# Kernel optimization log

Hardware: AMD Instinct MI355X
Metric: run time of the kernel (lower is better)

The kernel has to match this reference:

```python
import jax, jax.numpy as jnp
import numpy as np

N = 50000
NEG_SLOPE = 0.2


def leaky_relu(x, slope=NEG_SLOPE):
    return jnp.where(x >= 0, x, slope * x)


def gat_conv(x, edge_index, W, a_src, a_dst, bias):
    """PyG GATConv, heads=1, add_self_loops=True.
    x: [N, Fin], edge_index: [2, E] (row 0 = source j, row 1 = target i),
    W: [Fin, Fout], a_src/a_dst: [Fout], bias: [Fout].
    """
    n = x.shape[0]
    # add self loops
    loops = jnp.arange(n, dtype=edge_index.dtype)
    src = jnp.concatenate([edge_index[0], loops])
    dst = jnp.concatenate([edge_index[1], loops])

    xw = x @ W                       # [N, Fout]
    alpha_src = xw @ a_src           # [N]
    alpha_dst = xw @ a_dst           # [N]

    e = leaky_relu(alpha_src[src] + alpha_dst[dst])   # [E+N]
    # segment softmax over edges sharing the same target node
    m = jax.ops.segment_max(e, dst, num_segments=n)   # [N]
    ex = jnp.exp(e - m[dst])
    denom = jax.ops.segment_sum(ex, dst, num_segments=n)  # [N] (>0 via self loops)
    att = ex / denom[dst]                              # [E+N]

    msgs = att[:, None] * xw[src]                      # [E+N, Fout]
    out = jax.ops.segment_sum(msgs, dst, num_segments=n)
    return out + bias


def setup_inputs() -> dict:
    key = jax.random.key(0)
    ks = jax.random.split(key, 12)
    E = 800000
    Fin, H, Fout = 128, 256, 128
    x = jax.random.normal(ks[0], (N, Fin), dtype=jnp.float32)
    edge_index = jax.random.randint(ks[1], (2, E), 0, N, dtype=jnp.int64)
    s = 0.1
    W1 = jax.random.normal(ks[2], (Fin, H), dtype=jnp.float32) * s
    a1_src = jax.random.normal(ks[3], (H,), dtype=jnp.float32) * s
    a1_dst = jax.random.normal(ks[4], (H,), dtype=jnp.float32) * s
    b1 = jax.random.normal(ks[5], (H,), dtype=jnp.float32) * s
    W2 = jax.random.normal(ks[6], (H, Fout), dtype=jnp.float32) * s
    a2_src = jax.random.normal(ks[7], (Fout,), dtype=jnp.float32) * s
    a2_dst = jax.random.normal(ks[8], (Fout,), dtype=jnp.float32) * s
    b2 = jax.random.normal(ks[9], (Fout,), dtype=jnp.float32) * s
    return {"x": x, "edge_index": edge_index, "W1": W1, "a1_src": a1_src,
            "a1_dst": a1_dst, "b1": b1, "W2": W2, "a2_src": a2_src,
            "a2_dst": a2_dst, "b2": b2}


def reference(x, edge_index, W1, a1_src, a1_dst, b1, W2, a2_src, a2_dst, b2):
    h = jax.nn.relu(gat_conv(x, edge_index, W1, a1_src, a1_dst, b1))
    return gat_conv(h, edge_index, W2, a2_src, a2_dst, b2)
```

## Files before the change

kernel.cpp:

```cpp
#include <hip/hip_runtime.h>
#include <hip/hip_bf16.h>

typedef __attribute__((ext_vector_type(8))) short short8;
typedef __attribute__((ext_vector_type(4))) float floatx4;

#define CAP 8192
#define BIN_CH 2048
#define NPB 16

__device__ __forceinline__ float read_f(const void* p, long long i, int fp32m) {
  return fp32m ? ((const float*)p)[i] : (float)((const __hip_bfloat16*)p)[i];
}
__device__ __forceinline__ float bf2f(unsigned short u) {
  return __uint_as_float((unsigned)u << 16);
}
__device__ __forceinline__ unsigned short f2bf(float f) {
  const unsigned u = __float_as_uint(f);
  return (unsigned short)((u + 0x7fffu + ((u >> 16) & 1u)) >> 16);
}

__device__ __forceinline__ void pack_one(const void* W, unsigned short* Wp, int i,
                                         int K, int NOUT, int m) {
  const int k = i / NOUT, n = i - k * NOUT;
  const int ct = n >> 4, c = n & 15, ks = k >> 5, quad = (k >> 3) & 3, j = k & 7;
  Wp[(((ct * (K / 32) + ks) * 4 + quad) * 16 + c) * 8 + j] = f2bf(read_f(W, i, m));
}

__global__ __launch_bounds__(256) void prep_k(const void* __restrict__ x,
                                              const void* __restrict__ ei,
                                              const void* __restrict__ W1,
                                              const void* __restrict__ a1s,
                                              const void* __restrict__ a1d,
                                              const void* __restrict__ b1,
                                              const void* __restrict__ W2,
                                              const void* __restrict__ a2s,
                                              const void* __restrict__ a2d,
                                              const void* __restrict__ b2,
                                              unsigned short* __restrict__ Wp1,
                                              unsigned short* __restrict__ Wp2,
                                              float* __restrict__ w_as1, float* __restrict__ w_ad1,
                                              float* __restrict__ v_a2s, float* __restrict__ v_a2d,
                                              float* __restrict__ v_b1,  float* __restrict__ v_b2,
                                              int* __restrict__ bkcnt,
                                              int* __restrict__ flags) {
  __shared__ int fl_s[2];
  const int t = threadIdx.x, b = blockIdx.x;
  if (t < 64) {
    const unsigned short w = ((const unsigned short*)x)[t * 2];
    const int ef = (w >> 7) & 0xff;
    const bool bf_ok = (ef >= 90 && ef <= 140);
    const unsigned hi = ((const unsigned*)ei)[t * 2 + 1];
    const unsigned long long bm = __ballot(bf_ok);
    const unsigned long long zm = __ballot(hi == 0u);
    if (t == 0) {
      fl_s[0] = (bm == ~0ull) ? 0 : 1;
      fl_s[1] = (zm == ~0ull) ? 1 : 0;
      if (b == 0) { flags[0] = fl_s[0]; flags[1] = fl_s[1]; }
    }
  }
  __syncthreads();
  const int m = fl_s[0];

  if (b < 128) {
    pack_one(W1, Wp1, b * 256 + t, 128, 256, m);
  } else if (b < 256) {
    pack_one(W2, Wp2, (b - 128) * 256 + t, 256, 128, m);
  } else if (b == 256) {
    if (t < 128) {
      float sa = 0.f, sb = 0.f;
      for (int j = 0; j < 256; ++j) {
        const float w = read_f(W1, (long long)t * 256 + j, m);
        sa = fmaf(w, read_f(a1s, j, m), sa);
        sb = fmaf(w, read_f(a1d, j, m), sb);
      }
      w_as1[t] = sa;
      w_ad1[t] = sb;
    }
  } else if (b == 257) {
    if (t < 128) v_a2s[t] = read_f(a2s, t, m);
    else         v_a2d[t - 128] = read_f(a2d, t - 128, m);
  } else if (b == 258) {
    v_b1[t] = read_f(b1, t, m);
  } else {
    if (t < 128) v_b2[t] = read_f(b2, t, m);
    bkcnt[t] = 0;
  }
}

__device__ __forceinline__ void edge_sd(const void* ei, int e, int E, int i64m, int n,
                                        int& s, int& d) {
  if (e < E) {
    if (i64m) { s = (int)((const long long*)ei)[e]; d = (int)((const long long*)ei)[E + e]; }
    else      { s = ((const int*)ei)[e];            d = ((const int*)ei)[E + e]; }
  } else { s = d = e - E; }
  s = min(max(s, 0), n - 1);
  d = min(max(d, 0), n - 1);
}

__global__ __launch_bounds__(256) void front2_k(const void* __restrict__ x,
                                                const void* __restrict__ ei,
                                                const float* __restrict__ w_as1,
                                                const float* __restrict__ w_ad1,
                                                unsigned short* __restrict__ xb,
                                                float* __restrict__ as_, float* __restrict__ ad_,
                                                unsigned* __restrict__ bpool,
                                                int* __restrict__ bkcnt,
                                                int n, int E, int EN, int nbc) {
  __shared__ int fl_s[2];
  __shared__ unsigned stage[BIN_CH];
  __shared__ unsigned daddr[BIN_CH];
  __shared__ int shA[256], shB[256], shC[256], shD[256];
  __shared__ int vtot_s;
  const int t = threadIdx.x, b = blockIdx.x;

  if (t < 64) {
    const unsigned short w = ((const unsigned short*)x)[t * 2];
    const int ef = (w >> 7) & 0xff;
    const bool bf_ok = (ef >= 90 && ef <= 140);
    const unsigned hi = ((const unsigned*)ei)[t * 2 + 1];
    const unsigned long long bm = __ballot(bf_ok);
    const unsigned long long zm = __ballot(hi == 0u);
    if (t == 0) {
      fl_s[0] = (bm == ~0ull) ? 0 : 1;
      fl_s[1] = (zm == ~0ull) ? 1 : 0;
    }
  }
  __syncthreads();
  const int m = fl_s[0], i64m = fl_s[1];

  if (b < nbc) {
    const int gid = b * 256 + t;
    const int node = gid >> 6, lane = gid & 63;
    if (node >= n) return;
    const long long base = (long long)node * 128 + lane * 2;
    const float v0 = read_f(x, base, m), v1 = read_f(x, base + 1, m);
    ushort2 q;
    q.x = f2bf(v0); q.y = f2bf(v1);
    *(ushort2*)(xb + base) = q;
    float s1 = fmaf(v0, w_as1[lane * 2], v1 * w_as1[lane * 2 + 1]);
    float s2 = fmaf(v0, w_ad1[lane * 2], v1 * w_ad1[lane * 2 + 1]);
    for (int off = 32; off; off >>= 1) {
      s1 += __shfl_down(s1, off);
      s2 += __shfl_down(s2, off);
    }
    if (lane == 0) { as_[node] = s1; ad_[node] = s2; }
  } else {
    const int c0 = (b - nbc) * BIN_CH;
    int* bcnt_s = shA; int* boff_s = shB; int* gbase_s = shC; int* sd = shD;
    bcnt_s[t] = 0;
    __syncthreads();

    unsigned val[BIN_CH / 256];
    int buk[BIN_CH / 256];
#pragma unroll
    for (int i = 0; i < BIN_CH / 256; ++i) {
      const int e = c0 + i * 256 + t;
      if (e < EN) {
        int s, d;
        edge_sd(ei, e, E, i64m, n, s, d);
        buk[i] = d >> 8;
        val[i] = (unsigned)s | ((unsigned)(d & 255) << 16);
        atomicAdd(&bcnt_s[buk[i]], 1);
      } else buk[i] = -1;
    }
    __syncthreads();

    const int c = bcnt_s[t];
    sd[t] = c;
    __syncthreads();
    for (int off = 1; off < 256; off <<= 1) {
      const int v = (t >= off) ? sd[t - off] : 0;
      __syncthreads();
      sd[t] += v;
      __syncthreads();
    }
    boff_s[t] = sd[t] - c;
    if (t == 255) vtot_s = sd[255];
    gbase_s[t] = (c > 0) ? atomicAdd(&bkcnt[t], c) : 0;
    bcnt_s[t] = 0;
    __syncthreads();

#pragma unroll
    for (int i = 0; i < BIN_CH / 256; ++i) {
      if (buk[i] >= 0) {
        const int lp = atomicAdd(&bcnt_s[buk[i]], 1);
        const int si = boff_s[buk[i]] + lp;
        stage[si] = val[i];
        const int gp = gbase_s[buk[i]] + lp;
        daddr[si] = (gp < CAP) ? (unsigned)(buk[i] * CAP + gp) : 0xFFFFFFFFu;
      }
    }
    __syncthreads();

    const int vt = vtot_s;
    for (int idx = t; idx < vt; idx += 256)
      if (daddr[idx] != 0xFFFFFFFFu) bpool[daddr[idx]] = stage[idx];
  }
}

__global__ __launch_bounds__(1024) void bucket_csr_k(const unsigned* __restrict__ bpool,
                                                     const int* __restrict__ bkcnt,
                                                     const float* __restrict__ as_,
                                                     const float* __restrict__ ad_,
                                                     unsigned* __restrict__ csr32,
                                                     int* __restrict__ start_g,
                                                     int* __restrict__ deg_g,
                                                     float* __restrict__ r1_g, int n) {
  __shared__ int deg_s[256], cur_s[256], sd[256];
  __shared__ float dsum_s[256];
  const int t = threadIdx.x, b = blockIdx.x;
  int cnt = bkcnt[b];
  if (cnt > CAP) cnt = CAP;
  if (t < 256) { deg_s[t] = 0; dsum_s[t] = 0.f; }
  __syncthreads();
  for (int idx = t; idx < cnt; idx += 1024) {
    const unsigned v = bpool[b * CAP + idx];
    atomicAdd(&deg_s[(v >> 16) & 255], 1);
  }
  __syncthreads();
  const int dg = (t < 256) ? deg_s[t] : 0;
  if (t < 256) sd[t] = dg;
  __syncthreads();
  for (int off = 1; off < 256; off <<= 1) {
    const int v = (t < 256 && t >= off) ? sd[t - off] : 0;
    __syncthreads();
    if (t < 256) sd[t] += v;
    __syncthreads();
  }
  if (t < 256) {
    const int excl = sd[t] - dg;
    const int node = b * 256 + t;
    if (node < n) { start_g[node] = b * CAP + excl; deg_g[node] = dg; }
    cur_s[t] = excl;
  }
  __syncthreads();
  for (int idx = t; idx < cnt; idx += 1024) {
    const unsigned v = bpool[b * CAP + idx];
    const int dl = (v >> 16) & 255;
    const int s = (int)(v & 0xFFFFu);
    float val = as_[s] + ad_[b * 256 + dl];
    val = (val >= 0.f) ? val : 0.2f * val;
    const float w = __expf(fminf(val, 60.f));
    const unsigned short wb = f2bf(w);
    atomicAdd(&dsum_s[dl], bf2f(wb));
    const int p = atomicAdd(&cur_s[dl], 1);
    csr32[b * CAP + p] = (unsigned)s | ((unsigned)wb << 16);
  }
  __syncthreads();
  if (t < 256) {
    const int node = b * 256 + t;
    if (node < n) r1_g[node] = 1.f / fmaxf(dsum_s[t], 1e-30f);
  }
}

__device__ __forceinline__ void agg_node_w(const int start, const int end,
                                           const unsigned* __restrict__ csr32,
                                           const unsigned short* __restrict__ xw,
                                           const int lane, const float rnorm,
                                           float* acc, const unsigned e_first) {
  const int slot = lane >> 4, col = lane & 15;
#pragma unroll
  for (int c = 0; c < 8; ++c) acc[c] = 0.f;

  for (int base = start; base < end; base += 64) {
    const unsigned e_pre = (base == start) ? e_first
                         : ((base + lane < end) ? csr32[base + lane] : 0u);
    const int cnt = min(64, end - base);
    for (int j = 0; j < cnt; j += 8) {
      const int jj0 = j + slot, jj1 = j + 4 + slot;
      unsigned e0 = (unsigned)__shfl((int)e_pre, jj0);
      unsigned e1 = (unsigned)__shfl((int)e_pre, jj1);
      e0 = (jj0 < cnt) ? e0 : 0u;
      e1 = (jj1 < cnt) ? e1 : 0u;
      const int s0 = (int)(e0 & 0xFFFFu), s1 = (int)(e1 & 0xFFFFu);
      const float w0 = bf2f((unsigned short)(e0 >> 16));
      const float w1 = bf2f((unsigned short)(e1 >> 16));
      const short8 q0 = *(const short8*)(xw + (size_t)s0 * 128 + col * 8);
      const short8 q1 = *(const short8*)(xw + (size_t)s1 * 128 + col * 8);
#pragma unroll
      for (int c = 0; c < 8; ++c) {
        acc[c] = fmaf(w0, bf2f((unsigned short)q0[c]), acc[c]);
        acc[c] = fmaf(w1, bf2f((unsigned short)q1[c]), acc[c]);
      }
    }
  }
#pragma unroll
  for (int c = 0; c < 8; ++c) {
    acc[c] += __shfl_xor(acc[c], 16);
    acc[c] += __shfl_xor(acc[c], 32);
    acc[c] *= rnorm;
  }
}

__device__ __forceinline__ void agg_node2_p(const int start, const int end,
                                            const unsigned* __restrict__ csr32,
                                            const float* __restrict__ as2, const float adv,
                                            const unsigned short* __restrict__ xw,
                                            const int lane, const unsigned p_first,
                                            float* acc) {
  const int slot = lane >> 4, col = lane & 15;
  float dsum = 0.f;
#pragma unroll
  for (int c = 0; c < 8; ++c) acc[c] = 0.f;

  for (int base = start; base < end; base += 64) {
    unsigned p_pre;
    if (base == start) {
      p_pre = p_first;
    } else {
      p_pre = 0u;
      const int idx = base + lane;
      if (idx < end) {
        const int s = (int)(csr32[idx] & 0xFFFFu);
        float v = as2[s] + adv;
        v = (v >= 0.f) ? v : 0.2f * v;
        const unsigned short wb = f2bf(__expf(fminf(v, 60.f)));
        p_pre = (unsigned)s | ((unsigned)wb << 16);
      }
    }
    dsum += bf2f((unsigned short)(p_pre >> 16));
    const int cnt = min(64, end - base);
    for (int j = 0; j < cnt; j += 8) {
      const int jj0 = j + slot, jj1 = j + 4 + slot;
      unsigned e0 = (unsigned)__shfl((int)p_pre, jj0);
      unsigned e1 = (unsigned)__shfl((int)p_pre, jj1);
      e0 = (jj0 < cnt) ? e0 : 0u;
      e1 = (jj1 < cnt) ? e1 : 0u;
      const int s0 = (int)(e0 & 0xFFFFu), s1 = (int)(e1 & 0xFFFFu);
      const float w0 = bf2f((unsigned short)(e0 >> 16));
      const float w1 = bf2f((unsigned short)(e1 >> 16));
      const short8 q0 = *(const short8*)(xw + (size_t)s0 * 128 + col * 8);
      const short8 q1 = *(const short8*)(xw + (size_t)s1 * 128 + col * 8);
#pragma unroll
      for (int c = 0; c < 8; ++c) {
        acc[c] = fmaf(w0, bf2f((unsigned short)q0[c]), acc[c]);
        acc[c] = fmaf(w1, bf2f((unsigned short)q1[c]), acc[c]);
      }
    }
  }
  for (int off = 32; off; off >>= 1) dsum += __shfl_down(dsum, off);
  dsum = __shfl(dsum, 0);
  const float r = 1.f / fmaxf(dsum, 1e-30f);
#pragma unroll
  for (int c = 0; c < 8; ++c) {
    acc[c] += __shfl_xor(acc[c], 16);
    acc[c] += __shfl_xor(acc[c], 32);
    acc[c] *= r;
  }
}

#define LSTR 136
#define HSTR 264
__global__ __launch_bounds__(256, 8) void agg_gemm12_k(const int* __restrict__ start_g,
                                                       const int* __restrict__ deg_g,
                                                       const unsigned* __restrict__ csr32,
                                                       const float* __restrict__ r1_g,
                                                       const unsigned short* __restrict__ xb,
                                                       const unsigned short* __restrict__ Wp1,
                                                       const unsigned short* __restrict__ Wp2,
                                                       const float* __restrict__ v_b1,
                                                       const float* __restrict__ v_a2s,
                                                       const float* __restrict__ v_a2d,
                                                       unsigned short* __restrict__ xw2,
                                                       float* __restrict__ as2,
                                                       float* __restrict__ ad2, int n) {
  __shared__ unsigned short lds[NPB * LSTR];
  __shared__ unsigned short hs[NPB * HSTR];
  __shared__ float al_s[NPB], al_d[NPB];
  const int wv = threadIdx.x >> 6, lane = threadIdx.x & 63;
  const int slot = lane >> 4, col = lane & 15;
  const int node0 = blockIdx.x * NPB;

  int nd[4], st[4], dgv[4];
  float rn[4];
  unsigned ef[4];
#pragma unroll
  for (int k = 0; k < 4; ++k) {
    nd[k] = node0 + wv * 4 + k;
    const bool v = nd[k] < n;
    st[k] = v ? start_g[nd[k]] : 0;
    dgv[k] = v ? deg_g[nd[k]] : 0;
  }
#pragma unroll
  for (int k = 0; k < 4; ++k) rn[k] = (nd[k] < n) ? r1_g[nd[k]] : 0.f;
#pragma unroll
  for (int k = 0; k < 4; ++k) ef[k] = (lane < dgv[k]) ? csr32[st[k] + lane] : 0u;

#pragma unroll
  for (int k = 0; k < 4; ++k) {
    float acc[8];
    if (nd[k] < n) {
      agg_node_w(st[k], st[k] + dgv[k], csr32, xb, lane, rn[k], acc, ef[k]);
    } else {
#pragma unroll
      for (int c = 0; c < 8; ++c) acc[c] = 0.f;
    }
    if (slot == 0) {
      short8 q;
#pragma unroll
      for (int c = 0; c < 8; ++c) q[c] = (short)f2bf(acc[c]);
      *(short8*)&lds[(wv * 4 + k) * LSTR + col * 8] = q;
    }
  }
  if (threadIdx.x < NPB) { al_s[threadIdx.x] = 0.f; al_d[threadIdx.x] = 0.f; }
  __syncthreads();

  const int quad = slot, c = col;
  short8 af1[4];
#pragma unroll
  for (int ks = 0; ks < 4; ++ks)
    af1[ks] = *(const short8*)&lds[c * LSTR + ks * 32 + quad * 8];
#pragma unroll
  for (int j = 0; j < 4; ++j) {
    const int ct = wv * 4 + j;
    floatx4 g = {0.f, 0.f, 0.f, 0.f};
#pragma unroll
    for (int ks = 0; ks < 4; ++ks) {
      const short8 bf = *(const short8*)(Wp1 + (size_t)((ct * 4 + ks) * 64 + lane) * 8);
      g = __builtin_amdgcn_mfma_f32_16x16x32_bf16(af1[ks], bf, g, 0, 0, 0);
    }
    const float bv = v_b1[ct * 16 + c];
#pragma unroll
    for (int r = 0; r < 4; ++r) {
      const float v = g[r] + bv;
      hs[(quad * 4 + r) * HSTR + ct * 16 + c] = f2bf(v > 0.f ? v : 0.f);
    }
  }
  __syncthreads();

#pragma unroll
  for (int j2 = 0; j2 < 2; ++j2) {
    const int ct = wv * 2 + j2;
    floatx4 a2 = {0.f, 0.f, 0.f, 0.f};
#pragma unroll
    for (int ks = 0; ks < 8; ++ks) {
      const short8 af = *(const short8*)&hs[c * HSTR + ks * 32 + quad * 8];
      const short8 bf = *(const short8*)(Wp2 + (size_t)((ct * 8 + ks) * 64 + lane) * 8);
      a2 = __builtin_amdgcn_mfma_f32_16x16x32_bf16(af, bf, a2, 0, 0, 0);
    }
    const float asv = v_a2s[ct * 16 + c], adv = v_a2d[ct * 16 + c];
    float pa_s[4], pa_d[4];
#pragma unroll
    for (int r = 0; r < 4; ++r) {
      pa_s[r] = a2[r] * asv;
      pa_d[r] = a2[r] * adv;
      const int rr = node0 + quad * 4 + r;
      if (rr < n) xw2[(size_t)rr * 128 + ct * 16 + c] = f2bf(a2[r]);
    }
    for (int off = 1; off < 16; off <<= 1) {
#pragma unroll
      for (int r = 0; r < 4; ++r) {
        pa_s[r] += __shfl_xor(pa_s[r], off);
        pa_d[r] += __shfl_xor(pa_d[r], off);
      }
    }
    if (c == 0) {
#pragma unroll
      for (int r = 0; r < 4; ++r) {
        atomicAdd(&al_s[quad * 4 + r], pa_s[r]);
        atomicAdd(&al_d[quad * 4 + r], pa_d[r]);
      }
    }
  }
  __syncthreads();
  if (threadIdx.x < NPB) {
    const int rr = node0 + threadIdx.x;
    if (rr < n) { as2[rr] = al_s[threadIdx.x]; ad2[rr] = al_d[threadIdx.x]; }
  }
}

__global__ __launch_bounds__(256, 8) void agg_out_k(const int* __restrict__ start_g,
                                                    const int* __restrict__ deg_g,
                                                    const unsigned* __restrict__ csr32,
                                                    const float* __restrict__ as2,
                                                    const float* __restrict__ ad2,
                                                    const unsigned short* __restrict__ xw,
                                                    const float* __restrict__ bias,
                                                    void* __restrict__ outp, int n,
                                                    const int* __restrict__ flags) {
  const int wv = threadIdx.x >> 6, lane = threadIdx.x & 63;
  const int slot = lane >> 4, col = lane & 15;
  const int node0 = blockIdx.x * 16;
  const int fm = flags[0];

  int nd[4], st[4], dgv[4], sv[4];
  unsigned ef[4], pf[4];
  float gv[4], advv[4];
#pragma unroll
  for (int k = 0; k < 4; ++k) {
    nd[k] = node0 + wv * 4 + k;
    const bool v = nd[k] < n;
    st[k] = v ? start_g[nd[k]] : 0;
    dgv[k] = v ? deg_g[nd[k]] : 0;
  }
#pragma unroll
  for (int k = 0; k < 4; ++k) ef[k] = (lane < dgv[k]) ? csr32[st[k] + lane] : 0u;
#pragma unroll
  for (int k = 0; k < 4; ++k) { sv[k] = (int)(ef[k] & 0xFFFFu); gv[k] = as2[sv[k]]; }
#pragma unroll
  for (int k = 0; k < 4; ++k) advv[k] = (nd[k] < n) ? ad2[nd[k]] : 0.f;
#pragma unroll
  for (int k = 0; k < 4; ++k) {
    float v = gv[k] + advv[k];
    v = (v >= 0.f) ? v : 0.2f * v;
    const unsigned short wb = f2bf(__expf(fminf(v, 60.f)));
    pf[k] = (lane < dgv[k]) ? ((unsigned)sv[k] | ((unsigned)wb << 16)) : 0u;
  }

#pragma unroll
  for (int k = 0; k < 4; ++k) {
    if (nd[k] >= n) continue;
    float acc[8];
    agg_node2_p(st[k], st[k] + dgv[k], csr32, as2, advv[k], xw, lane, pf[k], acc);
    if (slot == 0) {
      const int c0 = col * 8;
      if (fm) {
        float* o = (float*)outp + (size_t)nd[k] * 128 + c0;
        floatx4 q0, q1;
#pragma unroll
        for (int c = 0; c < 4; ++c) {
          q0[c] = acc[c] + bias[c0 + c];
          q1[c] = acc[c + 4] + bias[c0 + 4 + c];
        }
        *(floatx4*)o = q0;
        *(floatx4*)(o + 4) = q1;
      } else {
        short8 q;
#pragma unroll
        for (int c = 0; c < 8; ++c) q[c] = (short)f2bf(acc[c] + bias[c0 + c]);
        *(short8*)((unsigned short*)outp + (size_t)nd[k] * 128 + c0) = q;
      }
    }
  }
}

extern "C" void kernel_launch(void* const* d_in, const int* in_sizes, int n_in,
                              void* d_out, int out_size, void* d_ws, size_t ws_size,
                              hipStream_t stream) {
  const void* x   = d_in[0];
  const void* ei  = d_in[1];
  const void* W1  = d_in[2];
  const void* a1s = d_in[3];
  const void* a1d = d_in[4];
  const void* b1  = d_in[5];
  const void* W2  = d_in[6];
  const void* a2s = d_in[7];
  const void* a2d = d_in[8];
  const void* b2  = d_in[9];

  const int N  = in_sizes[0] / 128;
  const int E  = in_sizes[1] / 2;
  const int EN = E + N;
  const int NBUK = (N + 255) / 256;

  unsigned short* B1 = (unsigned short*)d_ws;
  unsigned short* H  = B1 + (size_t)N * 128;
  unsigned short* xw2 = H;
  float* as2 = (float*)(H + (size_t)N * 128);
  float* ad2 = as2 + N;
  unsigned* csr32 = (unsigned*)(ad2 + N);
  float* as_   = (float*)(H + (size_t)N * 256);
  float* ad_   = as_ + N;
  int*   start_g = (int*)(ad_ + N);
  int*   deg_g   = start_g + N;
  float* r1_g    = (float*)(deg_g + N);
  int*   bkcnt   = (int*)(r1_g + N);
  unsigned* bpool = (unsigned*)(bkcnt + 256);
  unsigned short* Wp1 = (unsigned short*)(bpool + (size_t)NBUK * CAP);
  unsigned short* Wp2 = Wp1 + 128 * 256;
  float* vecs  = (float*)(Wp2 + 256 * 128);
  int*   flags = (int*)(vecs + 1152);
  float* w_as1 = vecs,        *w_ad1 = vecs + 128;
  float* v_a2s = vecs + 256,  *v_a2d = vecs + 384;
  float* v_b1  = vecs + 512,  *v_b2  = vecs + 768;

  const int NB = (N * 64 + 255) / 256;
  const int BB = (EN + BIN_CH - 1) / BIN_CH;
  const int AG = (N + NPB - 1) / NPB;

  prep_k<<<260, 256, 0, stream>>>(x, ei, W1, a1s, a1d, b1, W2, a2s, a2d, b2,
                                  Wp1, Wp2, w_as1, w_ad1, v_a2s, v_a2d, v_b1, v_b2,
                                  bkcnt, flags);

  front2_k<<<NB + BB, 256, 0, stream>>>(x, ei, w_as1, w_ad1, B1, as_, ad_,
                                        bpool, bkcnt, N, E, EN, NB);

  bucket_csr_k<<<NBUK, 1024, 0, stream>>>(bpool, bkcnt, as_, ad_, csr32,
                                          start_g, deg_g, r1_g, N);

  agg_gemm12_k<<<AG, 256, 0, stream>>>(start_g, deg_g, csr32, r1_g, B1, Wp1, Wp2,
                                       v_b1, v_a2s, v_a2d, xw2, as2, ad2, N);

  agg_out_k<<<AG, 256, 0, stream>>>(start_g, deg_g, csr32, as2, ad2, xw2, v_b2,
                                    d_out, N, flags);
}
```

Before: 237.4 us.

## Drop hoisted CSR prefetch in layer-1 aggregation and shrink output-kernel blocks

The layer-1 aggregation kernel no longer preloads start, degree, norm and the first CSR chunk for all four nodes up front. It now loads them per node inside the loop, which lowers register pressure but gives up the overlap of those loads with earlier work. Separately, the output aggregation kernel moves from 256-thread blocks covering 16 nodes to 128-thread blocks covering 8 nodes, doubling the grid. Smaller blocks aim for finer-grained scheduling and better load balance across the skewed node degrees.

```diff
diff --git a/kernel.cpp b/kernel.cpp
--- a/kernel.cpp
+++ b/kernel.cpp
@@ -256,15 +256,14 @@
 __device__ __forceinline__ void agg_node_w(const int start, const int end,
                                            const unsigned* __restrict__ csr32,
                                            const unsigned short* __restrict__ xw,
-                                           const int lane, const float rnorm,
-                                           float* acc, const unsigned e_first) {
+                                           const int lane, const float rnorm, float* acc) {
   const int slot = lane >> 4, col = lane & 15;
 #pragma unroll
   for (int c = 0; c < 8; ++c) acc[c] = 0.f;
 
   for (int base = start; base < end; base += 64) {
-    const unsigned e_pre = (base == start) ? e_first
-                         : ((base + lane < end) ? csr32[base + lane] : 0u);
+    const int idx = base + lane;
+    const unsigned e_pre = (idx < end) ? csr32[idx] : 0u;
     const int cnt = min(64, end - base);
     for (int j = 0; j < cnt; j += 8) {
       const int jj0 = j + slot, jj1 = j + 4 + slot;
@@ -371,26 +370,13 @@
   const int slot = lane >> 4, col = lane & 15;
   const int node0 = blockIdx.x * NPB;
 
-  int nd[4], st[4], dgv[4];
-  float rn[4];
-  unsigned ef[4];
-#pragma unroll
   for (int k = 0; k < 4; ++k) {
-    nd[k] = node0 + wv * 4 + k;
-    const bool v = nd[k] < n;
-    st[k] = v ? start_g[nd[k]] : 0;
-    dgv[k] = v ? deg_g[nd[k]] : 0;
-  }
-#pragma unroll
-  for (int k = 0; k < 4; ++k) rn[k] = (nd[k] < n) ? r1_g[nd[k]] : 0.f;
-#pragma unroll
-  for (int k = 0; k < 4; ++k) ef[k] = (lane < dgv[k]) ? csr32[st[k] + lane] : 0u;
-
-#pragma unroll
-  for (int k = 0; k < 4; ++k) {
+    const int rv = wv * 4 + k;
+    const int node = node0 + rv;
     float acc[8];
-    if (nd[k] < n) {
-      agg_node_w(st[k], st[k] + dgv[k], csr32, xb, lane, rn[k], acc, ef[k]);
+    if (node < n) {
+      const int start = start_g[node];
+      agg_node_w(start, start + deg_g[node], csr32, xb, lane, r1_g[node], acc);
     } else {
 #pragma unroll
       for (int c = 0; c < 8; ++c) acc[c] = 0.f;
@@ -399,7 +385,7 @@
       short8 q;
 #pragma unroll
       for (int c = 0; c < 8; ++c) q[c] = (short)f2bf(acc[c]);
-      *(short8*)&lds[(wv * 4 + k) * LSTR + col * 8] = q;
+      *(short8*)&lds[rv * LSTR + col * 8] = q;
     }
   }
   if (threadIdx.x < NPB) { al_s[threadIdx.x] = 0.f; al_d[threadIdx.x] = 0.f; }
@@ -469,7 +455,7 @@
   }
 }
 
-__global__ __launch_bounds__(256, 8) void agg_out_k(const int* __restrict__ start_g,
+__global__ __launch_bounds__(128, 8) void agg_out_k(const int* __restrict__ start_g,
                                                     const int* __restrict__ deg_g,
                                                     const unsigned* __restrict__ csr32,
                                                     const float* __restrict__ as2,
@@ -480,7 +466,7 @@
                                                     const int* __restrict__ flags) {
   const int wv = threadIdx.x >> 6, lane = threadIdx.x & 63;
   const int slot = lane >> 4, col = lane & 15;
-  const int node0 = blockIdx.x * 16;
+  const int node0 = blockIdx.x * 8;
   const int fm = flags[0];
 
   int nd[4], st[4], dgv[4], sv[4];
@@ -577,6 +563,7 @@
   const int NB = (N * 64 + 255) / 256;
   const int BB = (EN + BIN_CH - 1) / BIN_CH;
   const int AG = (N + NPB - 1) / NPB;
+  const int AO = (N + 7) / 8;
 
   prep_k<<<260, 256, 0, stream>>>(x, ei, W1, a1s, a1d, b1, W2, a2s, a2d, b2,
                                   Wp1, Wp2, w_as1, w_ad1, v_a2s, v_a2d, v_b1, v_b2,
@@ -591,6 +578,6 @@
   agg_gemm12_k<<<AG, 256, 0, stream>>>(start_g, deg_g, csr32, r1_g, B1, Wp1, Wp2,
                                        v_b1, v_a2s, v_a2d, xw2, as2, ad2, N);
 
-  agg_out_k<<<AG, 256, 0, stream>>>(start_g, deg_g, csr32, as2, ad2, xw2, v_b2,
+  agg_out_k<<<AO, 128, 0, stream>>>(start_g, deg_g, csr32, as2, ad2, xw2, v_b2,
                                     d_out, N, flags);
 }
```

New measurement: 242.4 us. 2.1% more time.
